# Kernel optimization log

Hardware: AMD Instinct MI355X
Metric: run time of the kernel (lower is better)

Reference implementation:

```python
import jax, jax.numpy as jnp
import numpy as np

B, S, E, H = 2, 2048, 1024, 16
D = E // H

def setup_inputs() -> dict:
    key = jax.random.key(0)
    ks = jax.random.split(key, 5)
    return {
        "hidden_states": jax.random.normal(ks[0], (B, S, E), dtype=jnp.float32),
        "c_attn_w": jax.random.normal(ks[1], (E, 3 * E), dtype=jnp.float32) * 0.02,
        "c_attn_b": jax.random.normal(ks[2], (3 * E,), dtype=jnp.float32) * 0.02,
        "c_proj_w": jax.random.normal(ks[3], (E, E), dtype=jnp.float32) * 0.02,
        "c_proj_b": jax.random.normal(ks[4], (E,), dtype=jnp.float32) * 0.02,
    }

def reference(hidden_states, c_attn_w, c_attn_b, c_proj_w, c_proj_b):
    x = hidden_states                      # [B, S, E]
    b, s, _ = x.shape
    w_q, w_k, w_v = jnp.split(c_attn_w, 3, axis=1)   # each [E, E]
    q_b, k_b, v_b = jnp.split(c_attn_b, 3, axis=0)   # each [E]

    # value projection
    v = x @ w_v + v_b                                        # [B,S,E]
    v = v.reshape(b, s, H, D).transpose(0, 2, 1, 3)          # [B,H,S,D]

    # fused query: ((x Wq + qb) Wk^T + kb)
    q = (x @ w_q + q_b) @ w_k.T + k_b                        # [B,S,E]
    qh = q.reshape(b, s, H, D).transpose(0, 2, 1, 3)         # [B,H,S,D]

    # key side is RAW hidden states split per head
    kh = x.reshape(b, s, H, D).transpose(0, 2, 1, 3)         # [B,H,S,D]

    scale = 1.0 / jnp.float32(D) ** 0.5
    scores = jnp.einsum("bhqd,bhkd->bhqk",
                        qh.astype(jnp.float32),
                        kh.astype(jnp.float32)) * scale       # [B,H,S,S] fp32

    causal = jnp.tril(jnp.ones((s, s), dtype=bool))
    mask_value = jnp.finfo(jnp.float32).min
    scores = jnp.where(causal[None, None], scores, mask_value)

    probs = jax.nn.softmax(scores, axis=-1).astype(v.dtype)  # [B,H,S,S]

    out = jnp.einsum("bhqk,bhkd->bhqd", probs, v)            # [B,H,S,D]
    out = out.transpose(0, 2, 1, 3).reshape(b, s, E)         # [B,S,E]
    out = out @ c_proj_w + c_proj_b
    return out
```

## Files before the change

### kernel.cpp

```cpp
#include <hip/hip_runtime.h>

typedef __attribute__((ext_vector_type(8))) __bf16 bf16x8;
typedef __attribute__((ext_vector_type(4))) __bf16 bf16x4;
typedef __attribute__((ext_vector_type(4))) float f32x4;

typedef __attribute__((address_space(1))) void as1_void;
typedef __attribute__((address_space(3))) void as3_void;

__device__ __forceinline__ void gl_lds16(const void* g, void* l) {
    __builtin_amdgcn_global_load_lds((const as1_void*)g, (as3_void*)l, 16, 0, 0);
}

__device__ __forceinline__ const bf16x8* swz(const __bf16* base, int row, int chunk) {
    return (const bf16x8*)((const char*)base + row * 128 + ((chunk ^ (row & 7)) * 16));
}

#define QSCALE (0.125f * 1.44269504f)

__global__ __launch_bounds__(256) void prep_kernel(
    const float* __restrict__ x, const float* __restrict__ caw,
    const float* __restrict__ cab, const float* __restrict__ cpw,
    __bf16* __restrict__ xb, __bf16* __restrict__ wvt,
    __bf16* __restrict__ wkn, __bf16* __restrict__ wqn,
    __bf16* __restrict__ wpt, float* __restrict__ bqv)
{
    __shared__ float tile[32 * 33];
    int bid = blockIdx.x;
    int tid = threadIdx.x;
    if (bid < 1024) {
        int nt = bid >> 5, kt = bid & 31;
        int tx = tid & 31, ty = tid >> 5;
        int n0 = nt * 32, k0 = kt * 32;
#pragma unroll
        for (int i = 0; i < 4; ++i)
            tile[(ty + i * 8) * 33 + tx] = caw[(long)(k0 + ty + i * 8) * 3072 + 2048 + n0 + tx];
        __syncthreads();
#pragma unroll
        for (int i = 0; i < 4; ++i)
            wvt[(long)(n0 + ty + i * 8) * 1024 + k0 + tx] = (__bf16)tile[tx * 33 + ty + i * 8];
    } else if (bid < 2048) {
        int v = bid - 1024;
        int nt = v >> 5, kt = v & 31;
        int tx = tid & 31, ty = tid >> 5;
        int n0 = nt * 32, k0 = kt * 32;
#pragma unroll
        for (int i = 0; i < 4; ++i)
            tile[(ty + i * 8) * 33 + tx] = cpw[(long)(k0 + ty + i * 8) * 1024 + n0 + tx];
        __syncthreads();
#pragma unroll
        for (int i = 0; i < 4; ++i)
            wpt[(long)(n0 + ty + i * 8) * 1024 + k0 + tx] = (__bf16)tile[tx * 33 + ty + i * 8];
    } else if (bid < 3072) {
        int e = (bid - 2048) * 1024 + tid * 4;
        int n = e >> 10, k = e & 1023;
        float4 f = *(const float4*)(caw + (long)n * 3072 + 1024 + k);
        bf16x4 o = {(__bf16)f.x, (__bf16)f.y, (__bf16)f.z, (__bf16)f.w};
        *(bf16x4*)(wkn + e) = o;
    } else if (bid < 4096) {
        int e = (bid - 3072) * 1024 + tid * 4;
        int n = e >> 10, k = e & 1023;
        float4 f = *(const float4*)(caw + (long)n * 3072 + k);
        bf16x4 o = {(__bf16)f.x, (__bf16)f.y, (__bf16)f.z, (__bf16)f.w};
        *(bf16x4*)(wqn + e) = o;
    } else if (bid < 8192) {
        long e = (long)(bid - 4096) * 1024 + tid * 4;
        float4 f = *(const float4*)(x + e);
        bf16x4 o = {(__bf16)f.x, (__bf16)f.y, (__bf16)f.z, (__bf16)f.w};
        *(bf16x4*)(xb + e) = o;
    } else {
        for (int i = tid; i < 1024; i += 256)
            bqv[1024 + i] = cab[2048 + i];
    }
}

__global__ __launch_bounds__(256) void bias_q_kernel(
    const __bf16* __restrict__ wkn, const float* __restrict__ cab,
    float* __restrict__ bqv)
{
    const int wave = threadIdx.x >> 6, lane = threadIdx.x & 63;
    float qb[16];
#pragma unroll
    for (int u = 0; u < 2; ++u) {
        float4 a = *(const float4*)(cab + u * 512 + lane * 8);
        float4 b = *(const float4*)(cab + u * 512 + lane * 8 + 4);
        qb[u * 8 + 0] = a.x; qb[u * 8 + 1] = a.y; qb[u * 8 + 2] = a.z; qb[u * 8 + 3] = a.w;
        qb[u * 8 + 4] = b.x; qb[u * 8 + 5] = b.y; qb[u * 8 + 6] = b.z; qb[u * 8 + 7] = b.w;
    }
    for (int i = 0; i < 16; ++i) {
        int n = blockIdx.x * 64 + wave * 16 + i;
        float s = 0.f;
#pragma unroll
        for (int u = 0; u < 2; ++u) {
            bf16x8 w = *(const bf16x8*)(wkn + (long)n * 1024 + u * 512 + lane * 8);
#pragma unroll
            for (int r = 0; r < 8; ++r) s += (float)w[r] * qb[u * 8 + r];
        }
#pragma unroll
        for (int off = 1; off < 64; off <<= 1) s += __shfl_xor(s, off);
        if (lane == 0) bqv[n] = (s + cab[1024 + n]) * QSCALE;
    }
}

template <bool BF16OUT, int BN>
__global__ __launch_bounds__(256) void gemm_bt(
    const __bf16* __restrict__ A, int lda,
    const __bf16* __restrict__ B, int ldb,
    const float* __restrict__ bias,
    void* __restrict__ C, int ldc, int K, float oscale)
{
    constexpr int NT = BN / 32;
    __shared__ __bf16 As[128 * 32];
    __shared__ __bf16 Bs[BN * 32];
    const int tid = threadIdx.x;
    const int lane = tid & 63;
    const int wave = tid >> 6;
    const int quad = lane >> 4, l16 = lane & 15;
    const long m0 = (long)blockIdx.y * 128;
    const long n0 = (long)blockIdx.x * BN;
    const int wm = (wave >> 1) * 64, wn = (wave & 1) * (BN / 2);

    f32x4 acc[4][NT] = {};

    for (int k0 = 0; k0 < K; k0 += 32) {
#pragma unroll
        for (int c = tid; c < (128 + BN) * 4; c += 256) {
            int row = c >> 2, cc = c & 3;
            if (row < 128)
                gl_lds16(A + (m0 + row) * lda + k0 + cc * 8, As + c * 8);
            else
                gl_lds16(B + (n0 + row - 128) * ldb + k0 + cc * 8, Bs + (c - 512) * 8);
        }
        __syncthreads();
        bf16x8 af[4], bfr[NT];
#pragma unroll
        for (int i = 0; i < 4; ++i)
            af[i] = *(const bf16x8*)(As + (wm + i * 16 + l16) * 32 + quad * 8);
#pragma unroll
        for (int j = 0; j < NT; ++j)
            bfr[j] = *(const bf16x8*)(Bs + (wn + j * 16 + l16) * 32 + quad * 8);
#pragma unroll
        for (int i = 0; i < 4; ++i)
#pragma unroll
            for (int j = 0; j < NT; ++j)
                acc[i][j] = __builtin_amdgcn_mfma_f32_16x16x32_bf16(af[i], bfr[j], acc[i][j], 0, 0, 0);
        __syncthreads();
    }
#pragma unroll
    for (int i = 0; i < 4; ++i) {
        long row = m0 + wm + i * 16 + quad * 4;
#pragma unroll
        for (int j = 0; j < NT; ++j) {
            int col = (int)n0 + wn + j * 16 + l16;
            float bb = bias ? bias[col] : 0.f;
#pragma unroll
            for (int r = 0; r < 4; ++r) {
                float v = (acc[i][j][r] + bb) * oscale;
                if (BF16OUT)
                    ((__bf16*)C)[(row + r) * ldc + col] = (__bf16)v;
                else
                    ((float*)C)[(row + r) * ldc + col] = v;
            }
        }
    }
}

__global__ __launch_bounds__(256) void gemm_qv(
    const __bf16* __restrict__ A,
    const __bf16* __restrict__ B,
    const float* __restrict__ bias,
    __bf16* __restrict__ Qout,
    __bf16* __restrict__ VTout)
{
    __shared__ __bf16 smem[128 * 136];
    __bf16* As = smem;
    __bf16* Bs = smem + 4096;
    const int tid = threadIdx.x;
    const int lane = tid & 63;
    const int wave = tid >> 6;
    const int quad = lane >> 4, l16 = lane & 15;
    const long m0 = (long)blockIdx.y * 128;
    const long n0 = (long)blockIdx.x * 128;
    const int wm = (wave >> 1) * 64, wn = (wave & 1) * 64;

    f32x4 acc[4][4] = {};

    for (int k0 = 0; k0 < 1024; k0 += 32) {
#pragma unroll
        for (int c = tid; c < 1024; c += 256) {
            int row = c >> 2, cc = c & 3;
            if (row < 128)
                gl_lds16(A + (m0 + row) * 1024 + k0 + cc * 8, As + c * 8);
            else
                gl_lds16(B + (n0 + row - 128) * 1024 + k0 + cc * 8, Bs + (c - 512) * 8);
        }
        __syncthreads();
        bf16x8 af[4], bfr[4];
#pragma unroll
        for (int i = 0; i < 4; ++i)
            af[i] = *(const bf16x8*)(As + (wm + i * 16 + l16) * 32 + quad * 8);
#pragma unroll
        for (int j = 0; j < 4; ++j)
            bfr[j] = *(const bf16x8*)(Bs + (wn + j * 16 + l16) * 32 + quad * 8);
#pragma unroll
        for (int i = 0; i < 4; ++i)
#pragma unroll
            for (int j = 0; j < 4; ++j)
                acc[i][j] = __builtin_amdgcn_mfma_f32_16x16x32_bf16(af[i], bfr[j], acc[i][j], 0, 0, 0);
        __syncthreads();
    }

    if (n0 < 1024) {
#pragma unroll
        for (int i = 0; i < 4; ++i) {
            long row = m0 + wm + i * 16 + quad * 4;
#pragma unroll
            for (int j = 0; j < 4; ++j) {
                int col = (int)n0 + wn + j * 16 + l16;
                float bb = bias[col];
#pragma unroll
                for (int r = 0; r < 4; ++r)
                    Qout[(row + r) * 1024 + col] = (__bf16)(acc[i][j][r] + bb);
            }
        }
    } else {
#pragma unroll
        for (int i = 0; i < 4; ++i) {
#pragma unroll
            for (int j = 0; j < 4; ++j) {
                int col = (int)n0 + wn + j * 16 + l16;
                float bb = bias[col];
                bf16x4 v;
#pragma unroll
                for (int r = 0; r < 4; ++r) v[r] = (__bf16)(acc[i][j][r] + bb);
                *(bf16x4*)(smem + (wn + j * 16 + l16) * 136 + wm + i * 16 + quad * 4) = v;
            }
        }
        __syncthreads();
        const int d0 = (int)n0 - 1024;
        const int bb = (int)(m0 >> 11);
        const int sl = (int)(m0 & 2047);
#pragma unroll
        for (int pass = 0; pass < 16; ++pass) {
            int idx = pass * 256 + tid;
            int n = idx >> 5;
            int mc = (idx & 31) * 4;
            bf16x4 v = *(const bf16x4*)(smem + n * 136 + mc);
            *(bf16x4*)(VTout + ((long)(bb * 1024 + d0 + n)) * 2048 + sl + mc) = v;
        }
    }
}

__global__ __launch_bounds__(256) void attn_kernel(
    const __bf16* __restrict__ Q,
    const __bf16* __restrict__ Xb,
    const __bf16* __restrict__ VT,
    __bf16* __restrict__ O)
{
    __shared__ __bf16 Ks[2 * 8192];
    __shared__ __bf16 Vs[2 * 8192];
    __shared__ __bf16 Ps[4 * 1024];
    const int tid = threadIdx.x;
    const int lane = tid & 63;
    const int wave = tid >> 6;
    const int quad = lane >> 4, l16 = lane & 15;
    const int qa = blockIdx.x;
    const int qb = 31 - qa;
    const int bh = blockIdx.y;
    const int b = bh >> 4, h = bh & 15;
    const long rowbase = (long)b * 2048;

    const int s0 = tid, s1 = tid + 256;
    const int c0 = ((s0 & 7) ^ ((s0 >> 3) & 7)) * 8;
    const int c1 = ((s1 & 7) ^ ((s1 >> 3) & 7)) * 8;

    bf16x8 ones;
#pragma unroll
    for (int i = 0; i < 8; ++i) ones[i] = (__bf16)1.0f;

    bf16x8 qfr[2][2];
#pragma unroll
    for (int t = 0; t < 2; ++t) {
        int qt = t ? qb : qa;
        const __bf16* qp = Q + (rowbase + qt * 64 + wave * 16 + l16) * 1024 + h * 64 + quad * 8;
        qfr[t][0] = *(const bf16x8*)(qp);
        qfr[t][1] = *(const bf16x8*)(qp + 32);
    }

    auto stage_tile = [&](int j, int buf, int sub) {
        __bf16* kd = Ks + buf * 8192 + sub * 4096;
        __bf16* vd = Vs + buf * 8192 + sub * 4096;
        gl_lds16(Xb + (rowbase + j * 64 + (s0 >> 3)) * 1024 + h * 64 + c0, kd + s0 * 8);
        gl_lds16(Xb + (rowbase + j * 64 + (s1 >> 3)) * 1024 + h * 64 + c1, kd + s1 * 8);
        gl_lds16(VT + ((long)(b * 1024 + h * 64 + (s0 >> 3))) * 2048 + j * 64 + c0, vd + s0 * 8);
        gl_lds16(VT + ((long)(b * 1024 + h * 64 + (s1 >> 3))) * 2048 + j * 64 + c1, vd + s1 * 8);
    };
    stage_tile(0, 0, 0);
    stage_tile(1, 0, 1);

    const int nouter = (qb + 2) >> 1;

    f32x4 oacc[2][4] = {};
    f32x4 lacc[2] = {};
    __bf16* Pw = Ps + wave * 1024;

    for (int jj = 0; jj < nouter; ++jj) {
        __syncthreads();
        if (jj + 1 < nouter) {
            stage_tile(2 * jj + 2, (jj + 1) & 1, 0);
            stage_tile(2 * jj + 3, (jj + 1) & 1, 1);
        }

#pragma unroll
        for (int sub = 0; sub < 2; ++sub) {
            const int j = 2 * jj + sub;
            if (j > qb) break;
            const __bf16* Kb = Ks + (jj & 1) * 8192 + sub * 4096;
            const __bf16* Vb = Vs + (jj & 1) * 8192 + sub * 4096;

            bf16x8 kf[2][4], vf[2][4];
#pragma unroll
            for (int kk = 0; kk < 2; ++kk)
#pragma unroll
                for (int kt = 0; kt < 4; ++kt) {
                    kf[kk][kt] = *swz(Kb, kt * 16 + l16, kk * 4 + quad);
                    vf[kk][kt] = *swz(Vb, kt * 16 + l16, kk * 4 + quad);
                }

#pragma unroll
            for (int t = 0; t < 2; ++t) {
                if (t == 0 && j > qa) continue;
                const int qt = t ? qb : qa;

                f32x4 sacc[4] = {};
#pragma unroll
                for (int kk = 0; kk < 2; ++kk)
#pragma unroll
                    for (int kt = 0; kt < 4; ++kt)
                        sacc[kt] = __builtin_amdgcn_mfma_f32_16x16x32_bf16(
                            kf[kk][kt], qfr[t][kk], sacc[kt], 0, 0, 0);

                if (j == qt) {
                    const int qloc = wave * 16 + l16;
#pragma unroll
                    for (int kt = 0; kt < 4; ++kt) {
                        bf16x4 pk;
#pragma unroll
                        for (int r = 0; r < 4; ++r) {
                            float s = sacc[kt][r];
                            if (kt * 16 + quad * 4 + r > qloc) s = -1e30f;
                            pk[r] = (__bf16)exp2f(s);
                        }
                        *(bf16x4*)((char*)Pw + l16 * 128 +
                                   (((kt * 2 + (quad >> 1)) ^ (l16 & 7)) * 16) + (quad & 1) * 8) = pk;
                    }
                } else {
#pragma unroll
                    for (int kt = 0; kt < 4; ++kt) {
                        bf16x4 pk;
#pragma unroll
                        for (int r = 0; r < 4; ++r)
                            pk[r] = (__bf16)exp2f(sacc[kt][r]);
                        *(bf16x4*)((char*)Pw + l16 * 128 +
                                   (((kt * 2 + (quad >> 1)) ^ (l16 & 7)) * 16) + (quad & 1) * 8) = pk;
                    }
                }

#pragma unroll
                for (int kk = 0; kk < 2; ++kk) {
                    bf16x8 pf = *swz(Pw, l16, kk * 4 + quad);
                    lacc[t] = __builtin_amdgcn_mfma_f32_16x16x32_bf16(ones, pf, lacc[t], 0, 0, 0);
#pragma unroll
                    for (int dt = 0; dt < 4; ++dt)
                        oacc[t][dt] = __builtin_amdgcn_mfma_f32_16x16x32_bf16(
                            vf[kk][dt], pf, oacc[t][dt], 0, 0, 0);
                }
            }
        }
    }

#pragma unroll
    for (int t = 0; t < 2; ++t) {
        const int qt = t ? qb : qa;
        float inv = 1.0f / lacc[t][0];
        long row = rowbase + qt * 64 + wave * 16 + l16;
#pragma unroll
        for (int dt = 0; dt < 4; ++dt) {
            bf16x4 ov;
#pragma unroll
            for (int r = 0; r < 4; ++r) ov[r] = (__bf16)(oacc[t][dt][r] * inv);
            *(bf16x4*)(O + row * 1024 + h * 64 + dt * 16 + quad * 4) = ov;
        }
    }
}

extern "C" void kernel_launch(void* const* d_in, const int* in_sizes, int n_in,
                              void* d_out, int out_size, void* d_ws, size_t ws_size,
                              hipStream_t stream) {
    const float* x   = (const float*)d_in[0];
    const float* caw = (const float*)d_in[1];
    const float* cab = (const float*)d_in[2];
    const float* cpw = (const float*)d_in[3];
    const float* cpb = (const float*)d_in[4];

    char* p = (char*)d_ws;
    auto alloc = [&](size_t bytes) {
        void* r = (void*)p;
        p += (bytes + 255) & ~(size_t)255;
        return r;
    };
    __bf16* xb    = (__bf16*)alloc(4096UL * 1024 * 2);
    __bf16* mtb   = (__bf16*)alloc(1024UL * 1024 * 2);
    __bf16* wvt   = (__bf16*)alloc(1024UL * 1024 * 2);
    __bf16* wkn   = (__bf16*)alloc(1024UL * 1024 * 2);
    __bf16* wqn   = (__bf16*)alloc(1024UL * 1024 * 2);
    __bf16* wpt   = (__bf16*)alloc(1024UL * 1024 * 2);
    float*  bqv   = (float*) alloc(2048UL * 4);
    __bf16* qbuf  = (__bf16*)alloc(4096UL * 1024 * 2);
    __bf16* vt    = (__bf16*)alloc(2048UL * 2048 * 2);
    __bf16* attn  = (__bf16*)alloc(4096UL * 1024 * 2);

    prep_kernel<<<8193, 256, 0, stream>>>(x, caw, cab, cpw, xb, wvt, wkn, wqn, wpt, bqv);

    bias_q_kernel<<<16, 256, 0, stream>>>(wkn, cab, bqv);
    gemm_bt<true, 64><<<dim3(16, 8), 256, 0, stream>>>(wkn, 1024, wqn, 1024, nullptr,
                                                       (void*)mtb, 1024, 1024, QSCALE);
    gemm_qv<<<dim3(16, 32), 256, 0, stream>>>(xb, mtb, bqv, qbuf, vt);
    attn_kernel<<<dim3(16, 32), 256, 0, stream>>>(qbuf, xb, vt, attn);
    gemm_bt<false, 64><<<dim3(16, 32), 256, 0, stream>>>(attn, 1024, wpt, 1024, cpb,
                                                         d_out, 1024, 1024, 1.0f);
    (void)in_sizes; (void)n_in; (void)out_size; (void)ws_size;
}
```

Measured before the change: 215.1 us.

## Fold q-bias into prep kernel, deepen GEMM K-tiles with swizzled LDS, remap attention grid

The separate bias_q kernel is merged into extra blocks of the prep kernel, which read the fp32 weights directly, saving one launch. Both GEMM kernels now stage 64-wide K slices per iteration with an XOR-swizzled LDS layout, halving barrier count and reducing bank conflicts. The attention grid swaps its axes so consecutive blocks share a query tile across heads, and the staging addresses are hoisted out of the loop. The small mtb GEMM uses BN=32 to launch more blocks; gemm_qv adds a barrier before reusing shared memory in its V-transpose epilogue.

```diff
diff --git a/kernel.cpp b/kernel.cpp
--- a/kernel.cpp
+++ b/kernel.cpp
@@ -68,36 +68,29 @@
         bf16x4 o = {(__bf16)f.x, (__bf16)f.y, (__bf16)f.z, (__bf16)f.w};
         *(bf16x4*)(xb + e) = o;
     } else {
-        for (int i = tid; i < 1024; i += 256)
-            bqv[1024 + i] = cab[2048 + i];
-    }
-}
-
-__global__ __launch_bounds__(256) void bias_q_kernel(
-    const __bf16* __restrict__ wkn, const float* __restrict__ cab,
-    float* __restrict__ bqv)
-{
-    const int wave = threadIdx.x >> 6, lane = threadIdx.x & 63;
-    float qb[16];
-#pragma unroll
-    for (int u = 0; u < 2; ++u) {
-        float4 a = *(const float4*)(cab + u * 512 + lane * 8);
-        float4 b = *(const float4*)(cab + u * 512 + lane * 8 + 4);
-        qb[u * 8 + 0] = a.x; qb[u * 8 + 1] = a.y; qb[u * 8 + 2] = a.z; qb[u * 8 + 3] = a.w;
-        qb[u * 8 + 4] = b.x; qb[u * 8 + 5] = b.y; qb[u * 8 + 6] = b.z; qb[u * 8 + 7] = b.w;
-    }
-    for (int i = 0; i < 16; ++i) {
-        int n = blockIdx.x * 64 + wave * 16 + i;
-        float s = 0.f;
-#pragma unroll
-        for (int u = 0; u < 2; ++u) {
-            bf16x8 w = *(const bf16x8*)(wkn + (long)n * 1024 + u * 512 + lane * 8);
-#pragma unroll
-            for (int r = 0; r < 8; ++r) s += (float)w[r] * qb[u * 8 + r];
-        }
-#pragma unroll
-        for (int off = 1; off < 64; off <<= 1) s += __shfl_xor(s, off);
-        if (lane == 0) bqv[n] = (s + cab[1024 + n]) * QSCALE;
+        int k = bid - 8192;
+        int wave = tid >> 6, lane = tid & 63;
+        float qv[16];
+#pragma unroll
+        for (int u = 0; u < 4; ++u) {
+            float4 q4 = *(const float4*)(cab + u * 256 + lane * 4);
+            qv[u * 4 + 0] = q4.x; qv[u * 4 + 1] = q4.y;
+            qv[u * 4 + 2] = q4.z; qv[u * 4 + 3] = q4.w;
+        }
+        for (int i = 0; i < 16; ++i) {
+            int n = k * 64 + wave * 16 + i;
+            float s = 0.f;
+#pragma unroll
+            for (int u = 0; u < 4; ++u) {
+                float4 w4 = *(const float4*)(caw + (long)n * 3072 + 1024 + u * 256 + lane * 4);
+                s += w4.x * qv[u * 4 + 0] + w4.y * qv[u * 4 + 1]
+                   + w4.z * qv[u * 4 + 2] + w4.w * qv[u * 4 + 3];
+            }
+#pragma unroll
+            for (int off = 1; off < 64; off <<= 1) s += __shfl_xor(s, off);
+            if (lane == 0) bqv[n] = (s + cab[1024 + n]) * QSCALE;
+        }
+        if (tid < 64) bqv[1024 + k * 64 + tid] = cab[2048 + k * 64 + tid];
     }
 }
 
@@ -109,8 +102,8 @@
     void* __restrict__ C, int ldc, int K, float oscale)
 {
     constexpr int NT = BN / 32;
-    __shared__ __bf16 As[128 * 32];
-    __shared__ __bf16 Bs[BN * 32];
+    __shared__ __bf16 As[128 * 64];
+    __shared__ __bf16 Bs[BN * 64];
     const int tid = threadIdx.x;
     const int lane = tid & 63;
     const int wave = tid >> 6;
@@ -121,28 +114,31 @@
 
     f32x4 acc[4][NT] = {};
 
-    for (int k0 = 0; k0 < K; k0 += 32) {
-#pragma unroll
-        for (int c = tid; c < (128 + BN) * 4; c += 256) {
-            int row = c >> 2, cc = c & 3;
+    for (int k0 = 0; k0 < K; k0 += 64) {
+#pragma unroll
+        for (int c = tid; c < (128 + BN) * 8; c += 256) {
+            int row = c >> 3, cc = (c & 7) ^ (row & 7);
             if (row < 128)
                 gl_lds16(A + (m0 + row) * lda + k0 + cc * 8, As + c * 8);
             else
-                gl_lds16(B + (n0 + row - 128) * ldb + k0 + cc * 8, Bs + (c - 512) * 8);
-        }
-        __syncthreads();
-        bf16x8 af[4], bfr[NT];
-#pragma unroll
-        for (int i = 0; i < 4; ++i)
-            af[i] = *(const bf16x8*)(As + (wm + i * 16 + l16) * 32 + quad * 8);
-#pragma unroll
-        for (int j = 0; j < NT; ++j)
-            bfr[j] = *(const bf16x8*)(Bs + (wn + j * 16 + l16) * 32 + quad * 8);
-#pragma unroll
-        for (int i = 0; i < 4; ++i)
+                gl_lds16(B + (n0 + row - 128) * ldb + k0 + cc * 8, Bs + (c - 1024) * 8);
+        }
+        __syncthreads();
+#pragma unroll
+        for (int kk = 0; kk < 2; ++kk) {
+            bf16x8 af[4], bfr[NT];
+#pragma unroll
+            for (int i = 0; i < 4; ++i)
+                af[i] = *swz(As, wm + i * 16 + l16, kk * 4 + quad);
 #pragma unroll
             for (int j = 0; j < NT; ++j)
-                acc[i][j] = __builtin_amdgcn_mfma_f32_16x16x32_bf16(af[i], bfr[j], acc[i][j], 0, 0, 0);
+                bfr[j] = *swz(Bs, wn + j * 16 + l16, kk * 4 + quad);
+#pragma unroll
+            for (int i = 0; i < 4; ++i)
+#pragma unroll
+                for (int j = 0; j < NT; ++j)
+                    acc[i][j] = __builtin_amdgcn_mfma_f32_16x16x32_bf16(af[i], bfr[j], acc[i][j], 0, 0, 0);
+        }
         __syncthreads();
     }
 #pragma unroll
@@ -173,7 +169,7 @@
 {
     __shared__ __bf16 smem[128 * 136];
     __bf16* As = smem;
-    __bf16* Bs = smem + 4096;
+    __bf16* Bs = smem + 8192;
     const int tid = threadIdx.x;
     const int lane = tid & 63;
     const int wave = tid >> 6;
@@ -184,28 +180,31 @@
 
     f32x4 acc[4][4] = {};
 
-    for (int k0 = 0; k0 < 1024; k0 += 32) {
-#pragma unroll
-        for (int c = tid; c < 1024; c += 256) {
-            int row = c >> 2, cc = c & 3;
+    for (int k0 = 0; k0 < 1024; k0 += 64) {
+#pragma unroll
+        for (int c = tid; c < 2048; c += 256) {
+            int row = c >> 3, cc = (c & 7) ^ (row & 7);
             if (row < 128)
                 gl_lds16(A + (m0 + row) * 1024 + k0 + cc * 8, As + c * 8);
             else
-                gl_lds16(B + (n0 + row - 128) * 1024 + k0 + cc * 8, Bs + (c - 512) * 8);
-        }
-        __syncthreads();
-        bf16x8 af[4], bfr[4];
-#pragma unroll
-        for (int i = 0; i < 4; ++i)
-            af[i] = *(const bf16x8*)(As + (wm + i * 16 + l16) * 32 + quad * 8);
-#pragma unroll
-        for (int j = 0; j < 4; ++j)
-            bfr[j] = *(const bf16x8*)(Bs + (wn + j * 16 + l16) * 32 + quad * 8);
-#pragma unroll
-        for (int i = 0; i < 4; ++i)
+                gl_lds16(B + (n0 + row - 128) * 1024 + k0 + cc * 8, Bs + (c - 1024) * 8);
+        }
+        __syncthreads();
+#pragma unroll
+        for (int kk = 0; kk < 2; ++kk) {
+            bf16x8 af[4], bfr[4];
+#pragma unroll
+            for (int i = 0; i < 4; ++i)
+                af[i] = *swz(As, wm + i * 16 + l16, kk * 4 + quad);
 #pragma unroll
             for (int j = 0; j < 4; ++j)
-                acc[i][j] = __builtin_amdgcn_mfma_f32_16x16x32_bf16(af[i], bfr[j], acc[i][j], 0, 0, 0);
+                bfr[j] = *swz(Bs, wn + j * 16 + l16, kk * 4 + quad);
+#pragma unroll
+            for (int i = 0; i < 4; ++i)
+#pragma unroll
+                for (int j = 0; j < 4; ++j)
+                    acc[i][j] = __builtin_amdgcn_mfma_f32_16x16x32_bf16(af[i], bfr[j], acc[i][j], 0, 0, 0);
+        }
         __syncthreads();
     }
 
@@ -223,6 +222,7 @@
             }
         }
     } else {
+        __syncthreads();
 #pragma unroll
         for (int i = 0; i < 4; ++i) {
 #pragma unroll
@@ -263,9 +263,9 @@
     const int lane = tid & 63;
     const int wave = tid >> 6;
     const int quad = lane >> 4, l16 = lane & 15;
-    const int qa = blockIdx.x;
+    const int qa = blockIdx.y;
     const int qb = 31 - qa;
-    const int bh = blockIdx.y;
+    const int bh = blockIdx.x;
     const int b = bh >> 4, h = bh & 15;
     const long rowbase = (long)b * 2048;
 
@@ -286,13 +286,18 @@
         qfr[t][1] = *(const bf16x8*)(qp + 32);
     }
 
+    const __bf16* kp0 = Xb + (rowbase + (s0 >> 3)) * 1024 + h * 64 + c0;
+    const __bf16* kp1 = Xb + (rowbase + (s1 >> 3)) * 1024 + h * 64 + c1;
+    const __bf16* vp0 = VT + ((long)(b * 1024 + h * 64 + (s0 >> 3))) * 2048 + c0;
+    const __bf16* vp1 = VT + ((long)(b * 1024 + h * 64 + (s1 >> 3))) * 2048 + c1;
+
     auto stage_tile = [&](int j, int buf, int sub) {
         __bf16* kd = Ks + buf * 8192 + sub * 4096;
         __bf16* vd = Vs + buf * 8192 + sub * 4096;
-        gl_lds16(Xb + (rowbase + j * 64 + (s0 >> 3)) * 1024 + h * 64 + c0, kd + s0 * 8);
-        gl_lds16(Xb + (rowbase + j * 64 + (s1 >> 3)) * 1024 + h * 64 + c1, kd + s1 * 8);
-        gl_lds16(VT + ((long)(b * 1024 + h * 64 + (s0 >> 3))) * 2048 + j * 64 + c0, vd + s0 * 8);
-        gl_lds16(VT + ((long)(b * 1024 + h * 64 + (s1 >> 3))) * 2048 + j * 64 + c1, vd + s1 * 8);
+        gl_lds16(kp0 + (long)j * 65536, kd + s0 * 8);
+        gl_lds16(kp1 + (long)j * 65536, kd + s1 * 8);
+        gl_lds16(vp0 + j * 64, vd + s0 * 8);
+        gl_lds16(vp1 + j * 64, vd + s1 * 8);
     };
     stage_tile(0, 0, 0);
     stage_tile(1, 0, 1);
@@ -419,13 +424,12 @@
     __bf16* vt    = (__bf16*)alloc(2048UL * 2048 * 2);
     __bf16* attn  = (__bf16*)alloc(4096UL * 1024 * 2);
 
-    prep_kernel<<<8193, 256, 0, stream>>>(x, caw, cab, cpw, xb, wvt, wkn, wqn, wpt, bqv);
-
-    bias_q_kernel<<<16, 256, 0, stream>>>(wkn, cab, bqv);
-    gemm_bt<true, 64><<<dim3(16, 8), 256, 0, stream>>>(wkn, 1024, wqn, 1024, nullptr,
+    prep_kernel<<<8208, 256, 0, stream>>>(x, caw, cab, cpw, xb, wvt, wkn, wqn, wpt, bqv);
+
+    gemm_bt<true, 32><<<dim3(32, 8), 256, 0, stream>>>(wkn, 1024, wqn, 1024, nullptr,
                                                        (void*)mtb, 1024, 1024, QSCALE);
     gemm_qv<<<dim3(16, 32), 256, 0, stream>>>(xb, mtb, bqv, qbuf, vt);
-    attn_kernel<<<dim3(16, 32), 256, 0, stream>>>(qbuf, xb, vt, attn);
+    attn_kernel<<<dim3(32, 16), 256, 0, stream>>>(qbuf, xb, vt, attn);
     gemm_bt<false, 64><<<dim3(16, 32), 256, 0, stream>>>(attn, 1024, wpt, 1024, cpb,
                                                          d_out, 1024, 1024, 1.0f);
     (void)in_sizes; (void)n_in; (void)out_size; (void)ws_size;
```

After: 188.3 us. -12.5%, faster.
